# Optimization experiments

Hardware: AMD Instinct MI355X
Metric: run time of the kernel (lower is better)

Reference implementation:

```python
import jax, jax.numpy as jnp
import numpy as np

N = 768
INPUT_DIM = 128
HIDDEN = 256
HEADS = 8
HEAD_DIM = HIDDEN // HEADS  # 32
SCALE = float(np.sqrt(HEAD_DIM))


def _linear_params(key, fan_in, fan_out):
    kw, kb = jax.random.split(key)
    lim = 1.0 / np.sqrt(fan_in)
    W = jax.random.uniform(kw, (fan_in, fan_out), jnp.float32, -lim, lim)
    b = jax.random.uniform(kb, (fan_out,), jnp.float32, -lim, lim)
    return W, b


def setup_inputs() -> dict:
    key = jax.random.key(0)
    ks = jax.random.split(key, 9)
    x = jax.random.normal(ks[0], (N, INPUT_DIM), jnp.float32)
    pos = jax.random.normal(ks[1], (N, 3), jnp.float32)
    Wq, bq = _linear_params(ks[2], INPUT_DIM, HIDDEN)
    Wk, bk = _linear_params(ks[3], INPUT_DIM, HIDDEN)
    Wv, bv = _linear_params(ks[4], INPUT_DIM, HIDDEN)
    Wo, bo = _linear_params(ks[5], HIDDEN, HIDDEN)
    W1, b1 = _linear_params(ks[6], 3, HIDDEN)
    W2, b2 = _linear_params(ks[7], HIDDEN, HIDDEN)
    W3, b3 = _linear_params(ks[8], HIDDEN, HEAD_DIM)
    return dict(x=x, pos=pos, Wq=Wq, bq=bq, Wk=Wk, bk=bk, Wv=Wv, bv=bv,
                Wo=Wo, bo=bo, W1=W1, b1=b1, W2=W2, b2=b2, W3=W3, b3=b3)


def reference(x, pos, Wq, bq, Wk, bk, Wv, bv, Wo, bo, W1, b1, W2, b2, W3, b3):
    n = x.shape[0]
    Q = (x @ Wq + bq).reshape(n, HEADS, HEAD_DIM)
    K = (x @ Wk + bk).reshape(n, HEADS, HEAD_DIM)
    V = (x @ Wv + bv).reshape(n, HEADS, HEAD_DIM)

    # rel_pos[i, j] = pos[j] - pos[i], shape (N, N, 3)
    rel = pos[None, :, :] - pos[:, None, :]
    h = jax.nn.relu(rel @ W1 + b1)          # (N, N, HIDDEN)
    h = jax.nn.relu(h @ W2 + b2)            # (N, N, HIDDEN)
    enc = h @ W3 + b3                        # (N, N, HEAD_DIM)

    scores = jnp.einsum('ihd,jhd->hij', Q, K) / SCALE
    scores = scores + jnp.einsum('ihd,ijd->hij', Q, enc) / SCALE
    attn = jax.nn.softmax(scores, axis=-1)   # (H, N, N); dropout is identity at eval
    out = jnp.einsum('hij,jhd->ihd', attn, V).reshape(n, HIDDEN)
    return out @ Wo + bo
```

## Files before the change

kernel.cpp:

```cpp
#include <hip/hip_runtime.h>
#include <hip/hip_bf16.h>

#define N 768
#define IN_DIM 128
#define HID 256
#define HD 32
#define TJ 64
#define NT (N / TJ)
#define NTH (NT / 2)
#define SCALE_INV 0.17677669529663687f

typedef short s16x8 __attribute__((ext_vector_type(8)));
typedef float f32x4 __attribute__((ext_vector_type(4)));

__device__ __forceinline__ float bf2f(unsigned short s) {
    return __uint_as_float(((unsigned)s) << 16);
}
__device__ __forceinline__ unsigned short bf_bits(float f) {
    __hip_bfloat16 h = __float2bfloat16(f);
    union { __hip_bfloat16 h; unsigned short u; } c; c.h = h; return c.u;
}
__device__ __forceinline__ unsigned cvt2(float a, float b) {
    __hip_bfloat162 h2 = __float22bfloat162_rn(make_float2(a, b));
    union { __hip_bfloat162 h; unsigned u; } c; c.h = h2; return c.u;
}

#define BAR_LDS() do { asm volatile("s_waitcnt lgkmcnt(0)" ::: "memory"); \
                       __builtin_amdgcn_s_barrier(); } while (0)

__global__ __launch_bounds__(256) void prep_kernel(
    const float* __restrict__ x, const float* __restrict__ pos,
    const float* __restrict__ Wq, const float* __restrict__ bq,
    const float* __restrict__ Wk, const float* __restrict__ bk,
    const float* __restrict__ Wv, const float* __restrict__ bv,
    const float* __restrict__ W1, const float* __restrict__ W2,
    const float* __restrict__ W3, const float* __restrict__ Wo,
    float* __restrict__ Q, float* __restrict__ Kt,
    unsigned short* __restrict__ Vt, float* __restrict__ A,
    unsigned short* __restrict__ w2f, float* __restrict__ WoT,
    unsigned short* __restrict__ w3qg)
{
    const int bx = blockIdx.x, t = threadIdx.x;
    __shared__ float xs[IN_DIM];
    __shared__ float ps[3];
    __shared__ float qrow[HID];

    if (bx >= N) {
        const int p = (bx - N) * 256 + t;
        const int e = p & 7, l = (p >> 3) & 63, nt = (p >> 9) & 15, s = p >> 13;
        const int krow = 32 * s + 8 * (l >> 4) + e;
        const int ncol = 16 * nt + (l & 15);
        w2f[p] = bf_bits(W2[krow * HID + ncol]);
        WoT[p] = Wo[(p & 255) * HID + (p >> 8)];
        return;
    }

    const int i = bx;
    if (t < IN_DIM) xs[t] = x[i * IN_DIM + t];
    if (t < 3) ps[t] = pos[i * 3 + t];
    __syncthreads();
    float q = bq[t], k = bk[t], v = bv[t];
#pragma unroll 8
    for (int kk = 0; kk < IN_DIM; ++kk) {
        const float xv = xs[kk];
        q += xv * Wq[kk * HID + t];
        k += xv * Wk[kk * HID + t];
        v += xv * Wv[kk * HID + t];
    }
    const float a = ps[0] * W1[t] + ps[1] * W1[HID + t] + ps[2] * W1[2 * HID + t];
    Q[i * HID + t] = q;
    Kt[(size_t)t * N + i] = k;
    Vt[(size_t)t * N + i] = bf_bits(v);
    A[i * HID + t] = a;
    qrow[t] = q;
    __syncthreads();

    const int l = t & 63, sp = t >> 6, lg = l >> 4, hh = l & 15;
#pragma unroll
    for (int ss = 0; ss < 2; ++ss) {
        const int s = 2 * sp + ss;
        s16x8 frag = {0, 0, 0, 0, 0, 0, 0, 0};
        if (hh < 8) {
#pragma unroll
            for (int e = 0; e < 8; ++e) {
                const int kk = 32 * s + 8 * lg + e;
                const float* w3p = W3 + kk * HD;
                float acc = 0.f;
#pragma unroll
                for (int d0 = 0; d0 < 32; d0 += 4) {
                    const float4 wv = *(const float4*)(w3p + d0);
                    acc += wv.x * qrow[hh * HD + d0] + wv.y * qrow[hh * HD + d0 + 1]
                         + wv.z * qrow[hh * HD + d0 + 2] + wv.w * qrow[hh * HD + d0 + 3];
                }
                frag[e] = (short)bf_bits(acc);
            }
        }
        *(s16x8*)(w3qg + (size_t)i * 4096 + (size_t)(s * 64 + l) * 8) = frag;
    }
}

__global__ __launch_bounds__(256) void s1_kernel(
    const float* __restrict__ Q, const float* __restrict__ Kt,
    float* __restrict__ S1)
{
    const int t = threadIdx.x;
    const int i0 = (blockIdx.x / 12) * 32;
    const int j0 = (blockIdx.x % 12) * 64;
    __shared__ float qTs[256 * 36];

    {
        const int iq = t & 31;
        const int dbase = (t >> 5) * 32;
        const int xk = t >> 5;
        const int colsw = (((iq >> 2) ^ xk) << 2) + (iq & 3);
        const float* qp = Q + (size_t)(i0 + iq) * HID + dbase;
#pragma unroll
        for (int cc = 0; cc < 8; ++cc) {
            const float4 qv = *(const float4*)(qp + 4 * cc);
            qTs[(dbase + 4 * cc + 0) * 36 + colsw] = qv.x;
            qTs[(dbase + 4 * cc + 1) * 36 + colsw] = qv.y;
            qTs[(dbase + 4 * cc + 2) * 36 + colsw] = qv.z;
            qTs[(dbase + 4 * cc + 3) * 36 + colsw] = qv.w;
        }
    }
    __syncthreads();

    const int h = t >> 5, jj = t & 31;
    const int j1 = j0 + jj, j2 = j0 + jj + 32;
    f32x4 acc0[8] = {}, acc1[8] = {};
    const float* kp = Kt + (size_t)(32 * h) * N + j1;
#pragma unroll 4
    for (int d = 0; d < 32; ++d) {
        const float k0 = kp[(size_t)d * N];
        const float k1 = kp[(size_t)d * N + 32];
        const float* qrow = &qTs[(32 * h + d) * 36];
#pragma unroll
        for (int ic = 0; ic < 8; ++ic) {
            const f32x4 qv = *(const f32x4*)&qrow[(ic ^ h) << 2];
            acc0[ic] += qv * k0;
            acc1[ic] += qv * k1;
        }
    }
    float* op = S1 + (size_t)h * (N * N) + (size_t)i0 * N;
#pragma unroll
    for (int ic = 0; ic < 8; ++ic)
#pragma unroll
        for (int u = 0; u < 4; ++u) {
            op[(size_t)(4 * ic + u) * N + j1] = acc0[ic][u];
            op[(size_t)(4 * ic + u) * N + j2] = acc1[ic][u];
        }
}

__global__ __launch_bounds__(256, 2) void fused_main_kernel(
    const float* __restrict__ Ag, const float* __restrict__ S1,
    const unsigned short* __restrict__ Vt,
    const unsigned short* __restrict__ w2fg, const unsigned short* __restrict__ w3qg,
    const float* __restrict__ b1, const float* __restrict__ b2,
    float* __restrict__ pv0g, float* __restrict__ pv1g,
    float* __restrict__ psump, float* __restrict__ mp)
{
    const int bid = blockIdx.x;
    const int i = bid >> 1, jh = bid & 1;
    const int t = threadIdx.x;
    const int w = t >> 6, l = t & 63;
    const int lg = l >> 4, l15 = l & 15;

    __shared__ __align__(16) short h1f[4 * 8 * 64 * 8];
    __shared__ __align__(16) short h2s[64 * 264];
    __shared__ __align__(16) short w3qf[8 * 64 * 8];
    __shared__ __align__(16) float slds[8 * 68];
    __shared__ __align__(16) float plds[8 * 68];
    __shared__ float basek[HID];
    __shared__ float hm[8], hpsum[8], hresc[8];

    basek[t] = b1[t] - Ag[(size_t)i * HID + t];
    {
        const int c0 = t, c1 = t + 256;
        *(s16x8*)&w3qf[c0 * 8] = *(const s16x8*)(w3qg + (size_t)i * 4096 + (size_t)c0 * 8);
        *(s16x8*)&w3qf[c1 * 8] = *(const s16x8*)(w3qg + (size_t)i * 4096 + (size_t)c1 * 8);
    }
    if (t < 8) { hm[t] = -3.0e38f; hpsum[t] = 0.f; }
    float bias[4];
#pragma unroll
    for (int n = 0; n < 4; ++n) bias[n] = b2[64 * w + 16 * n + l15];

    float pv = 0.f;
    const int h = t >> 5;
    const unsigned short* vrow = Vt + (size_t)t * N;
    BAR_LDS();

#pragma unroll 1
    for (int tt = 0; tt < NTH; ++tt) {
        const int j0 = (jh * NTH + tt) * TJ;

        const int jj = 16 * w + l15;
        const float* ap = Ag + (size_t)(j0 + jj) * HID + 8 * lg;
#pragma unroll
        for (int s = 0; s < 8; ++s) {
            const float4 a0 = *(const float4*)(ap + 32 * s);
            const float4 a1 = *(const float4*)(ap + 32 * s + 4);
            const float4 c0 = *(const float4*)&basek[32 * s + 8 * lg];
            const float4 c4 = *(const float4*)&basek[32 * s + 8 * lg + 4];
            uint4 hv;
            hv.x = cvt2(fmaxf(a0.x + c0.x, 0.f), fmaxf(a0.y + c0.y, 0.f));
            hv.y = cvt2(fmaxf(a0.z + c0.z, 0.f), fmaxf(a0.w + c0.w, 0.f));
            hv.z = cvt2(fmaxf(a1.x + c4.x, 0.f), fmaxf(a1.y + c4.y, 0.f));
            hv.w = cvt2(fmaxf(a1.z + c4.z, 0.f), fmaxf(a1.w + c4.w, 0.f));
            *(uint4*)&h1f[((w * 8 + s) * 64 + l) * 8] = hv;
        }
        s16x8 bfr[32];
#pragma unroll
        for (int s = 0; s < 8; ++s)
#pragma unroll
            for (int n = 0; n < 4; ++n)
                bfr[s * 4 + n] = *(const s16x8*)(w2fg +
                    (size_t)(((s * 16 + 4 * w + n) * 64 + l)) * 8);
        BAR_LDS();

#pragma unroll
        for (int mt = 0; mt < 4; ++mt) {
            s16x8 a[8];
#pragma unroll
            for (int s = 0; s < 8; ++s)
                a[s] = *(const s16x8*)&h1f[((mt * 8 + s) * 64 + l) * 8];
#pragma unroll
            for (int n = 0; n < 4; ++n) {
                f32x4 acc = {bias[n], bias[n], bias[n], bias[n]};
#pragma unroll
                for (int s = 0; s < 8; ++s)
                    acc = __builtin_amdgcn_mfma_f32_16x16x32_bf16(a[s], bfr[s * 4 + n], acc, 0, 0, 0);
                const int col = 64 * w + 16 * n + l15;
                const int jrow = 16 * mt + 4 * lg;
#pragma unroll
                for (int r = 0; r < 4; ++r)
                    h2s[(jrow + r) * 264 + col] = (short)bf_bits(fmaxf(acc[r], 0.f));
            }
        }
        BAR_LDS();

        float4 s1v = make_float4(0.f, 0.f, 0.f, 0.f);
        if (l15 < 8)
            s1v = *(const float4*)(S1 + (size_t)l15 * (N * N) + (size_t)i * N
                                   + j0 + 16 * w + 4 * lg);
        f32x4 acc2 = {};
#pragma unroll
        for (int s = 0; s < 8; ++s) {
            const s16x8 a2 = *(const s16x8*)&h2s[(16 * w + l15) * 264 + 32 * s + 8 * lg];
            const s16x8 wq = *(const s16x8*)&w3qf[(s * 64 + l) * 8];
            acc2 = __builtin_amdgcn_mfma_f32_16x16x32_bf16(a2, wq, acc2, 0, 0, 0);
        }
        if (l15 < 8) {
            float4 sc;
            sc.x = (acc2[0] + s1v.x) * SCALE_INV;
            sc.y = (acc2[1] + s1v.y) * SCALE_INV;
            sc.z = (acc2[2] + s1v.z) * SCALE_INV;
            sc.w = (acc2[3] + s1v.w) * SCALE_INV;
            *(float4*)&slds[l15 * 68 + 16 * w + 4 * lg] = sc;
        }
        BAR_LDS();

        {
            const int h0 = w, h1 = w + 4;
            const float s0 = slds[h0 * 68 + l];
            const float s1 = slds[h1 * 68 + l];
            float m0 = s0, m1 = s1;
#pragma unroll
            for (int o = 1; o < 64; o <<= 1) {
                m0 = fmaxf(m0, __shfl_xor(m0, o));
                m1 = fmaxf(m1, __shfl_xor(m1, o));
            }
            const float M0 = hm[h0], M1 = hm[h1];
            const float nm0 = fmaxf(M0, m0), nm1 = fmaxf(M1, m1);
            const float p0 = __expf(s0 - nm0), p1 = __expf(s1 - nm1);
            plds[h0 * 68 + l] = p0;
            plds[h1 * 68 + l] = p1;
            float t0 = p0, t1 = p1;
#pragma unroll
            for (int o = 1; o < 64; o <<= 1) {
                t0 += __shfl_xor(t0, o);
                t1 += __shfl_xor(t1, o);
            }
            if (l == 0) {
                const float r0 = __expf(M0 - nm0), r1 = __expf(M1 - nm1);
                hresc[h0] = r0; hresc[h1] = r1;
                hpsum[h0] = hpsum[h0] * r0 + t0;
                hpsum[h1] = hpsum[h1] * r1 + t1;
                hm[h0] = nm0; hm[h1] = nm1;
            }
        }
        BAR_LDS();

        {
            pv *= hresc[h];
            const unsigned short* vp = vrow + j0;
            const float* pp = &plds[h * 68];
#pragma unroll
            for (int c = 0; c < 8; ++c) {
                const s16x8 vv = *(const s16x8*)(vp + c * 8);
                const float4 pa = *(const float4*)(pp + 8 * c);
                const float4 pb = *(const float4*)(pp + 8 * c + 4);
                pv += pa.x * bf2f((unsigned short)vv[0]) + pa.y * bf2f((unsigned short)vv[1])
                    + pa.z * bf2f((unsigned short)vv[2]) + pa.w * bf2f((unsigned short)vv[3])
                    + pb.x * bf2f((unsigned short)vv[4]) + pb.y * bf2f((unsigned short)vv[5])
                    + pb.z * bf2f((unsigned short)vv[6]) + pb.w * bf2f((unsigned short)vv[7]);
            }
        }
    }

    float* pvb = jh ? pv1g : pv0g;
    pvb[(size_t)i * HID + t] = pv;
    if (t < 8) {
        psump[(size_t)bid * 8 + t] = hpsum[t];
        mp[(size_t)bid * 8 + t] = hm[t];
    }
}

__global__ __launch_bounds__(256) void combine_kernel(
    const float* __restrict__ pv0g, const float* __restrict__ pv1g,
    const float* __restrict__ psump, const float* __restrict__ mp,
    const float* __restrict__ WoT, const float* __restrict__ bo,
    float* __restrict__ out)
{
    const int i = blockIdx.x, t = threadIdx.x;
    const int h = t >> 5;
    __shared__ float oa[HID];

    const float m0 = mp[(size_t)(2 * i) * 8 + h];
    const float m1 = mp[(size_t)(2 * i + 1) * 8 + h];
    const float ms = fmaxf(m0, m1);
    const float e0 = __expf(m0 - ms), e1 = __expf(m1 - ms);
    const float num = pv0g[(size_t)i * HID + t] * e0 + pv1g[(size_t)i * HID + t] * e1;
    const float den = psump[(size_t)(2 * i) * 8 + h] * e0
                    + psump[(size_t)(2 * i + 1) * 8 + h] * e1;
    oa[t] = num / den;
    __syncthreads();

    float r = bo[t];
    const float* wop = WoT + (size_t)t * HID;
#pragma unroll 4
    for (int k = 0; k < HID; k += 4) {
        const float4 ov = *(const float4*)&oa[k];
        const float4 wv = *(const float4*)(wop + k);
        r += ov.x * wv.x + ov.y * wv.y + ov.z * wv.z + ov.w * wv.w;
    }
    out[(size_t)i * HID + t] = r;
}

extern "C" void kernel_launch(void* const* d_in, const int* in_sizes, int n_in,
                              void* d_out, int out_size, void* d_ws, size_t ws_size,
                              hipStream_t stream)
{
    const float* x   = (const float*)d_in[0];
    const float* pos = (const float*)d_in[1];
    const float* Wq  = (const float*)d_in[2];
    const float* bq  = (const float*)d_in[3];
    const float* Wk  = (const float*)d_in[4];
    const float* bk  = (const float*)d_in[5];
    const float* Wv  = (const float*)d_in[6];
    const float* bv  = (const float*)d_in[7];
    const float* Wo  = (const float*)d_in[8];
    const float* bo  = (const float*)d_in[9];
    const float* W1  = (const float*)d_in[10];
    const float* b1  = (const float*)d_in[11];
    const float* W2  = (const float*)d_in[12];
    const float* b2  = (const float*)d_in[13];
    const float* W3  = (const float*)d_in[14];
    const float* b3  = (const float*)d_in[15];
    (void)b3;
    float* out = (float*)d_out;

    char* ws = (char*)d_ws;
    float* Q  = (float*)(ws + 0);
    float* A  = (float*)(ws + 786432);
    float* Kt = (float*)(ws + 1572864);
    unsigned short* Vtb = (unsigned short*)(ws + 2359296);
    float* S1 = (float*)(ws + 2752512);
    unsigned short* w2f  = (unsigned short*)(ws + 21626880);
    unsigned short* w3qg = (unsigned short*)(ws + 21757952);
    float* WoT = (float*)(ws + 28049408);
    float* pv0g  = (float*)(ws + 0);
    float* pv1g  = (float*)(ws + 1572864);
    float* psump = (float*)(ws + 28311552);
    float* mp    = (float*)(ws + 28360704);

    prep_kernel<<<1024, 256, 0, stream>>>(x, pos, Wq, bq, Wk, bk, Wv, bv,
                                          W1, W2, W3, Wo,
                                          Q, Kt, Vtb, A, w2f, WoT, w3qg);
    s1_kernel<<<288, 256, 0, stream>>>(Q, Kt, S1);
    fused_main_kernel<<<2 * N, 256, 0, stream>>>(A, S1, Vtb, w2f, w3qg,
                                                 b1, b2, pv0g, pv1g, psump, mp);
    combine_kernel<<<N, 256, 0, stream>>>(pv0g, pv1g, psump, mp, WoT, bo, out);
}
```

Measured before the change: 211.9 us.

## Remap PV heads per wave to drop barrier and prefetch S1/V loads

Remaps each thread's PV output column so that every wave accumulates exactly the two heads whose softmax it computed. The post-softmax workgroup barrier can then become a wave-local LDS waitcnt. The S1 bias load is hoisted before the first MFMA stage, and the V row loads are issued before the softmax reductions to hide global-memory latency. A barrier is added at the end so the hpsum/hm reads stay correct, and the register pressure from the prefetched V vectors goes up.

```diff
diff --git a/kernel.cpp b/kernel.cpp
--- a/kernel.cpp
+++ b/kernel.cpp
@@ -160,7 +160,7 @@
     float* __restrict__ psump, float* __restrict__ mp)
 {
     const int bid = blockIdx.x;
-    const int i = bid >> 1, jh = bid & 1;
+    const int i = bid >> 1, jhalf = bid & 1;
     const int t = threadIdx.x;
     const int w = t >> 6, l = t & 63;
     const int lg = l >> 4, l15 = l & 15;
@@ -185,13 +185,14 @@
     for (int n = 0; n < 4; ++n) bias[n] = b2[64 * w + 16 * n + l15];
 
     float pv = 0.f;
-    const int h = t >> 5;
-    const unsigned short* vrow = Vt + (size_t)t * N;
+    const int hsel = w + ((l >> 5) << 2);
+    const int hid2 = hsel * 32 + (l & 31);
+    const unsigned short* vrow = Vt + (size_t)hid2 * N;
     BAR_LDS();
 
 #pragma unroll 1
     for (int tt = 0; tt < NTH; ++tt) {
-        const int j0 = (jh * NTH + tt) * TJ;
+        const int j0 = (jhalf * NTH + tt) * TJ;
 
         const int jj = 16 * w + l15;
         const float* ap = Ag + (size_t)(j0 + jj) * HID + 8 * lg;
@@ -208,6 +209,10 @@
             hv.w = cvt2(fmaxf(a1.z + c4.z, 0.f), fmaxf(a1.w + c4.w, 0.f));
             *(uint4*)&h1f[((w * 8 + s) * 64 + l) * 8] = hv;
         }
+        float4 s1v = make_float4(0.f, 0.f, 0.f, 0.f);
+        if (l15 < 8)
+            s1v = *(const float4*)(S1 + (size_t)l15 * (N * N) + (size_t)i * N
+                                   + j0 + 16 * w + 4 * lg);
         s16x8 bfr[32];
 #pragma unroll
         for (int s = 0; s < 8; ++s)
@@ -238,10 +243,6 @@
         }
         BAR_LDS();
 
-        float4 s1v = make_float4(0.f, 0.f, 0.f, 0.f);
-        if (l15 < 8)
-            s1v = *(const float4*)(S1 + (size_t)l15 * (N * N) + (size_t)i * N
-                                   + j0 + 16 * w + 4 * lg);
         f32x4 acc2 = {};
 #pragma unroll
         for (int s = 0; s < 8; ++s) {
@@ -259,6 +260,13 @@
         }
         BAR_LDS();
 
+        s16x8 vv[8];
+        {
+            const unsigned short* vp = vrow + j0;
+#pragma unroll
+            for (int c = 0; c < 8; ++c) vv[c] = *(const s16x8*)(vp + c * 8);
+        }
+
         {
             const int h0 = w, h1 = w + 4;
             const float s0 = slds[h0 * 68 + l];
@@ -288,27 +296,27 @@
                 hm[h0] = nm0; hm[h1] = nm1;
             }
         }
-        BAR_LDS();
+        asm volatile("s_waitcnt lgkmcnt(0)" ::: "memory");
 
         {
-            pv *= hresc[h];
-            const unsigned short* vp = vrow + j0;
-            const float* pp = &plds[h * 68];
+            pv *= hresc[hsel];
+            const float* pp = &plds[hsel * 68];
 #pragma unroll
             for (int c = 0; c < 8; ++c) {
-                const s16x8 vv = *(const s16x8*)(vp + c * 8);
+                const s16x8 vvv = vv[c];
                 const float4 pa = *(const float4*)(pp + 8 * c);
                 const float4 pb = *(const float4*)(pp + 8 * c + 4);
-                pv += pa.x * bf2f((unsigned short)vv[0]) + pa.y * bf2f((unsigned short)vv[1])
-                    + pa.z * bf2f((unsigned short)vv[2]) + pa.w * bf2f((unsigned short)vv[3])
-                    + pb.x * bf2f((unsigned short)vv[4]) + pb.y * bf2f((unsigned short)vv[5])
-                    + pb.z * bf2f((unsigned short)vv[6]) + pb.w * bf2f((unsigned short)vv[7]);
-            }
-        }
-    }
-
-    float* pvb = jh ? pv1g : pv0g;
-    pvb[(size_t)i * HID + t] = pv;
+                pv += pa.x * bf2f((unsigned short)vvv[0]) + pa.y * bf2f((unsigned short)vvv[1])
+                    + pa.z * bf2f((unsigned short)vvv[2]) + pa.w * bf2f((unsigned short)vvv[3])
+                    + pb.x * bf2f((unsigned short)vvv[4]) + pb.y * bf2f((unsigned short)vvv[5])
+                    + pb.z * bf2f((unsigned short)vvv[6]) + pb.w * bf2f((unsigned short)vvv[7]);
+            }
+        }
+    }
+
+    float* pvb = jhalf ? pv1g : pv0g;
+    pvb[(size_t)i * HID + hid2] = pv;
+    BAR_LDS();
     if (t < 8) {
         psump[(size_t)bid * 8 + t] = hpsum[t];
         mp[(size_t)bid * 8 + t] = hm[t];
```

New measurement: 209.3 us, median of 2. No clear change (-1.2%).
